# Kernel tuning notes

Measured on AMD Instinct MI355X. Metric: run time of the kernel, lower is better.

The kernel has to match this reference:

```python
import jax, jax.numpy as jnp
import numpy as np

N = 16384          # tokens (batch*seq)
D = 2048           # input_dim
H = 2 * D          # router hidden dim
E = 64             # num_experts
NUM_SHARED = 8
TOP_K = 2


def setup_inputs() -> dict:
    key = jax.random.key(0)
    k_x, k_w1, k_b1, k_w2, k_b2 = jax.random.split(key, 5)
    s1 = 1.0 / np.sqrt(D)
    s2 = 1.0 / np.sqrt(H)
    return {
        "x": jax.random.normal(k_x, (N, D), dtype=jnp.float32),
        "W1": jax.random.uniform(k_w1, (D, H), jnp.float32, -s1, s1),
        "b1": jax.random.uniform(k_b1, (H,), jnp.float32, -s1, s1),
        "W2": jax.random.uniform(k_w2, (H, E), jnp.float32, -s2, s2),
        "b2": jax.random.uniform(k_b2, (E,), jnp.float32, -s2, s2),
    }


def reference(x, W1, b1, W2, b2):
    # router MLP: linear -> exact (erf) GELU -> linear -> softmax
    h = jax.nn.gelu(x @ W1 + b1, approximate=False)          # [N, H]
    weights = jax.nn.softmax(h @ W2 + b2, axis=-1)            # [N, E]
    global_weights = weights[:, :NUM_SHARED]                  # [N, num_shared]
    local = weights[:, NUM_SHARED:]                           # [N, E - num_shared]
    local_weights, local_indices = jax.lax.top_k(local, TOP_K)  # [N, top_k] each
    return (global_weights, local_weights, local_indices, weights)
```

## Files before the change

### kernel.cpp

```cpp
#include <hip/hip_runtime.h>
#include <math.h>

namespace {
constexpr int kN = 16384;
constexpr int kD = 2048;
constexpr int kH = 4096;
constexpr int kE = 64;
constexpr int kShared = 8;

constexpr int OFF_GW = 0;
constexpr int OFF_LW = kN * kShared;
constexpr int OFF_LI = OFF_LW + kN * 2;
constexpr int OFF_W  = OFF_LI + kN * 2;

constexpr int GS_STRIDE = 132;
constexpr int HSPLIT = 4;
constexpr int CHUNKS = 8;

constexpr size_t XH_OFF  = 0;
constexpr size_t XL_OFF  = (size_t)kN * kD;
constexpr size_t W1TH_OFF = XL_OFF + (size_t)kN * kD;
constexpr size_t W1TL_OFF = W1TH_OFF + (size_t)kH * kD;
constexpr size_t WS_BASE = (W1TL_OFF + (size_t)kH * kD) * 2;
constexpr size_t PART_FLOAT_OFF = WS_BASE / 4;
constexpr size_t WS_FULL = WS_BASE + (size_t)HSPLIT * kN * kE * 4;

constexpr int BUF_FLOATS = 64 * GS_STRIDE;
constexpr int BUF_F16    = BUF_FLOATS * 2;
}

typedef _Float16 half8  __attribute__((ext_vector_type(8)));
typedef _Float16 half4t __attribute__((ext_vector_type(4)));
typedef float    f32x16 __attribute__((ext_vector_type(16)));

__device__ __forceinline__ void async16(const _Float16* g, _Float16* l) {
    __builtin_amdgcn_global_load_lds(
        (const __attribute__((address_space(1))) void*)g,
        (__attribute__((address_space(3))) void*)l, 16, 0, 0);
}

__global__ __launch_bounds__(256)
void convert_x(const float* __restrict__ x, _Float16* __restrict__ xh,
               _Float16* __restrict__ xl)
{
    const size_t i = ((size_t)blockIdx.x * 256 + threadIdx.x) * 4;
    const float4 v = *reinterpret_cast<const float4*>(x + i);
    half4t h, l;
    const float vs[4] = {v.x, v.y, v.z, v.w};
    #pragma unroll
    for (int j = 0; j < 4; ++j) {
        const _Float16 hj = (_Float16)vs[j];
        h[j] = hj;
        l[j] = (_Float16)((vs[j] - (float)hj) * 2048.0f);
    }
    *reinterpret_cast<half4t*>(xh + i) = h;
    *reinterpret_cast<half4t*>(xl + i) = l;
}

__global__ __launch_bounds__(256)
void convert_w1t(const float* __restrict__ W1, _Float16* __restrict__ th,
                 _Float16* __restrict__ tl)
{
    __shared__ float T[64][65];
    const int bk = blockIdx.x & 31;
    const int bn = blockIdx.x >> 5;
    const int k0 = bk * 64, n0 = bn * 64;
    const int t = threadIdx.x;
    const int c4 = (t & 15) * 4, r = t >> 4;

    #pragma unroll
    for (int i = 0; i < 4; ++i) {
        const int kk = r + 16 * i;
        const float4 v = *reinterpret_cast<const float4*>(
            W1 + (size_t)(k0 + kk) * kH + n0 + c4);
        T[kk][c4 + 0] = v.x; T[kk][c4 + 1] = v.y;
        T[kk][c4 + 2] = v.z; T[kk][c4 + 3] = v.w;
    }
    __syncthreads();
    #pragma unroll
    for (int i = 0; i < 4; ++i) {
        const int nn = r + 16 * i;
        half4t h, l;
        #pragma unroll
        for (int j = 0; j < 4; ++j) {
            const float vv = T[c4 + j][nn];
            const _Float16 hj = (_Float16)vv;
            h[j] = hj;
            l[j] = (_Float16)((vv - (float)hj) * 2048.0f);
        }
        *reinterpret_cast<half4t*>(th + (size_t)(n0 + nn) * kD + k0 + c4) = h;
        *reinterpret_cast<half4t*>(tl + (size_t)(n0 + nn) * kD + k0 + c4) = l;
    }
}

__global__ __launch_bounds__(256, 2)
void gemm1_mfma(const _Float16* __restrict__ xh, const float* __restrict__ b1,
                const float* __restrict__ W2, float* __restrict__ dst,
                int atomicMode)
{
    __shared__ __align__(16) float smem[2 * BUF_FLOATS];

    const int t = threadIdx.x;
    const int lane = t & 63;
    const int w = t >> 6;
    const int bx = blockIdx.x;
    const int hSplit = bx & 3;
    const int rowBlock = bx >> 2;
    const int rowBase = rowBlock * 128;

    const int mw = (w >> 1) * 64, nw = (w & 1) * 64;

    unsigned int gofsA[4], gofsB[4];
    #pragma unroll
    for (int i = 0; i < 8; ++i) {
        const int c = i * 256 + t;
        const int tile = c >> 9;
        const int s = c & 511;
        const int row = s >> 2;
        const int pq = s & 3;
        const int q = pq ^ (row & 3) ^ ((row >> 2) & 3);
        const unsigned int plane =
            (tile == 0) ? (unsigned int)XH_OFF :
            (tile == 1) ? (unsigned int)XL_OFF :
            (tile == 2) ? (unsigned int)W1TH_OFF : (unsigned int)W1TL_OFF;
        if (tile < 2)
            gofsA[i] = plane + (unsigned int)(rowBase + row) * kD + q * 8;
        else
            gofsB[i - 4] = plane + (unsigned int)row * kD + q * 8;
    }

    int aOff[2][2], bOff[2][2];
    #pragma unroll
    for (int mt = 0; mt < 2; ++mt)
        #pragma unroll
        for (int ks = 0; ks < 2; ++ks) {
            const int row = mw + mt * 32 + (lane & 31);
            const int q = (lane >> 5) + 2 * ks;
            aOff[mt][ks] = row * 32 + ((q ^ (row & 3) ^ ((row >> 2) & 3)) * 8);
        }
    #pragma unroll
    for (int nt = 0; nt < 2; ++nt)
        #pragma unroll
        for (int ks = 0; ks < 2; ++ks) {
            const int row = nw + nt * 32 + (lane & 31);
            const int q = (lane >> 5) + 2 * ks;
            bOff[nt][ks] = row * 32 + ((q ^ (row & 3) ^ ((row >> 2) & 3)) * 8);
        }

    const int g_r0 = (t >> 3) * 4;
    const int g_e0 = (t & 7) * 8;
    float lacc[4][8];
    #pragma unroll
    for (int i = 0; i < 4; ++i)
        #pragma unroll
        for (int j = 0; j < 8; ++j) lacc[i][j] = 0.0f;

    auto stage = [&](int buf, int chunk, int kt) {
        _Float16* l = (_Float16*)smem + (size_t)buf * BUF_F16;
        const unsigned int hOff =
            (unsigned int)(hSplit * (CHUNKS * 128) + chunk * 128) * kD;
        #pragma unroll
        for (int i = 0; i < 4; ++i)
            async16(xh + gofsA[i] + kt, l + ((i * 256 + t) * 8));
        #pragma unroll
        for (int i = 0; i < 4; ++i)
            async16(xh + gofsB[i] + hOff + kt, l + (((i + 4) * 256 + t) * 8));
    };

    int cur = 0;
    stage(0, 0, 0);

    for (int chunk = 0; chunk < CHUNKS; ++chunk) {
        const int hBase = hSplit * (CHUNKS * 128) + chunk * 128;

        f32x16 accH[2][2], accL[2][2];
        #pragma unroll
        for (int a = 0; a < 2; ++a)
            #pragma unroll
            for (int b = 0; b < 2; ++b)
                #pragma unroll
                for (int r = 0; r < 16; ++r) { accH[a][b][r] = 0.0f; accL[a][b][r] = 0.0f; }

        for (int kt = 0; kt < kD; kt += 32) {
            const bool isLast = (chunk == CHUNKS - 1) && (kt == kD - 32);
            if (!isLast) {
                int nc = chunk, nk = kt + 32;
                if (nk == kD) { nc = chunk + 1; nk = 0; }
                stage(cur ^ 1, nc, nk);
                asm volatile("s_waitcnt vmcnt(8)" ::: "memory");
            } else {
                asm volatile("s_waitcnt vmcnt(0)" ::: "memory");
            }
            __builtin_amdgcn_s_barrier();
            asm volatile("" ::: "memory");

            const _Float16* lds = (const _Float16*)smem + (size_t)cur * BUF_F16;

            half8 aH[2][2], aL[2][2], bH[2][2], bL[2][2];
            #pragma unroll
            for (int mt = 0; mt < 2; ++mt)
                #pragma unroll
                for (int ks = 0; ks < 2; ++ks) {
                    aH[mt][ks] = *reinterpret_cast<const half8*>(lds + aOff[mt][ks]);
                    aL[mt][ks] = *reinterpret_cast<const half8*>(lds + 4096 + aOff[mt][ks]);
                }
            #pragma unroll
            for (int nt = 0; nt < 2; ++nt)
                #pragma unroll
                for (int ks = 0; ks < 2; ++ks) {
                    bH[nt][ks] = *reinterpret_cast<const half8*>(lds + 8192 + bOff[nt][ks]);
                    bL[nt][ks] = *reinterpret_cast<const half8*>(lds + 12288 + bOff[nt][ks]);
                }

            #pragma unroll
            for (int ks = 0; ks < 2; ++ks)
                #pragma unroll
                for (int mt = 0; mt < 2; ++mt)
                    #pragma unroll
                    for (int nt = 0; nt < 2; ++nt) {
                        accH[mt][nt] = __builtin_amdgcn_mfma_f32_32x32x16_f16(
                            aH[mt][ks], bH[nt][ks], accH[mt][nt], 0, 0, 0);
                        accL[mt][nt] = __builtin_amdgcn_mfma_f32_32x32x16_f16(
                            aH[mt][ks], bL[nt][ks], accL[mt][nt], 0, 0, 0);
                        accL[mt][nt] = __builtin_amdgcn_mfma_f32_32x32x16_f16(
                            aL[mt][ks], bH[nt][ks], accL[mt][nt], 0, 0, 0);
                    }

            asm volatile("s_waitcnt lgkmcnt(0)" ::: "memory");
            __builtin_amdgcn_s_barrier();
            cur ^= 1;
        }

        float* gS = smem + (size_t)(cur ^ 1) * BUF_FLOATS;
        const float inv2048 = 1.0f / 2048.0f;
        for (int hf = 0; hf < 2; ++hf) {
            asm volatile("s_waitcnt lgkmcnt(0)" ::: "memory");
            __builtin_amdgcn_s_barrier();
            asm volatile("" ::: "memory");
            if ((w & 1) == hf) {
                #pragma unroll
                for (int nt = 0; nt < 2; ++nt) {
                    const int hl = nt * 32 + (lane & 31);
                    const float bb = b1[hBase + hf * 64 + hl];
                    #pragma unroll
                    for (int mt = 0; mt < 2; ++mt) {
                        #pragma unroll
                        for (int rq = 0; rq < 4; ++rq) {
                            float vr[4];
                            #pragma unroll
                            for (int rr = 0; rr < 4; ++rr) {
                                const int r = rq * 4 + rr;
                                const float hv = accH[mt][nt][r] + accL[mt][nt][r] * inv2048 + bb;
                                vr[rr] = 0.5f * hv * (1.0f + erff(hv * 0.70710678118654752f));
                            }
                            const int mrow = mw + mt * 32 + 8 * rq + 4 * (lane >> 5);
                            *reinterpret_cast<float4*>(gS + hl * GS_STRIDE + mrow) =
                                make_float4(vr[0], vr[1], vr[2], vr[3]);
                        }
                    }
                }
            }
            asm volatile("s_waitcnt lgkmcnt(0)" ::: "memory");
            __builtin_amdgcn_s_barrier();
            asm volatile("" ::: "memory");
            const float* W2p = W2 + (size_t)(hBase + hf * 64) * kE + g_e0;
            #pragma unroll 4
            for (int h = 0; h < 64; ++h) {
                const float4 gv = *reinterpret_cast<const float4*>(gS + h * GS_STRIDE + g_r0);
                const float4 w0 = *reinterpret_cast<const float4*>(W2p + (size_t)h * kE);
                const float4 w1 = *reinterpret_cast<const float4*>(W2p + (size_t)h * kE + 4);
                const float ga[4] = {gv.x, gv.y, gv.z, gv.w};
                const float wb[8] = {w0.x, w0.y, w0.z, w0.w, w1.x, w1.y, w1.z, w1.w};
                #pragma unroll
                for (int i = 0; i < 4; ++i)
                    #pragma unroll
                    for (int j = 0; j < 8; ++j)
                        lacc[i][j] = fmaf(ga[i], wb[j], lacc[i][j]);
            }
        }
        asm volatile("s_waitcnt lgkmcnt(0)" ::: "memory");
        __builtin_amdgcn_s_barrier();
    }

    if (atomicMode) {
        #pragma unroll
        for (int i = 0; i < 4; ++i)
            #pragma unroll
            for (int j = 0; j < 8; ++j)
                atomicAdd(dst + (size_t)(rowBase + g_r0 + i) * kE + g_e0 + j, lacc[i][j]);
    } else {
        float* drow = dst + ((size_t)hSplit * kN + rowBase + g_r0) * kE + g_e0;
        #pragma unroll
        for (int i = 0; i < 4; ++i) {
            *reinterpret_cast<float4*>(drow + (size_t)i * kE) =
                make_float4(lacc[i][0], lacc[i][1], lacc[i][2], lacc[i][3]);
            *reinterpret_cast<float4*>(drow + (size_t)i * kE + 4) =
                make_float4(lacc[i][4], lacc[i][5], lacc[i][6], lacc[i][7]);
        }
    }
}

__global__ __launch_bounds__(256, 2)
void gemm1_kernel(const float* __restrict__ x, const float* __restrict__ W1,
                  const float* __restrict__ b1, const float* __restrict__ W2,
                  float* __restrict__ logits)
{
    __shared__ __align__(16) float smem[64 * GS_STRIDE];
    float* As = smem;
    float* Bs = smem + 32 * 128;
    float* gS = smem;

    const int t  = threadIdx.x;
    const int bx = blockIdx.x;
    const int rowBlock = bx >> 2;
    const int hSplit   = bx & 3;
    const int rowBase  = rowBlock * 128;
    const int hBase0   = hSplit * 1024;

    const int ty = t >> 4;
    const int tx = t & 15;
    const int r0 = ty * 8;
    const int c0 = tx * 8;
    const int g_r0 = (t >> 3) * 4;
    const int g_e0 = (t & 7) * 8;

    float lacc[4][8];
    #pragma unroll
    for (int i = 0; i < 4; ++i)
        #pragma unroll
        for (int j = 0; j < 8; ++j) lacc[i][j] = 0.0f;

    for (int chunk = 0; chunk < 8; ++chunk) {
        const int hBase = hBase0 + chunk * 128;
        float C[8][8];
        #pragma unroll
        for (int i = 0; i < 8; ++i)
            #pragma unroll
            for (int j = 0; j < 8; ++j) C[i][j] = 0.0f;

        for (int kt = 0; kt < kD; kt += 32) {
            __syncthreads();
            #pragma unroll
            for (int i = 0; i < 4; ++i) {
                const int f  = t + 256 * i;
                const int m  = f >> 3;
                const int kq = (f & 7) * 4;
                const float4 v = *reinterpret_cast<const float4*>(
                    x + (size_t)(rowBase + m) * kD + kt + kq);
                As[(kq + 0) * 128 + m] = v.x;
                As[(kq + 1) * 128 + m] = v.y;
                As[(kq + 2) * 128 + m] = v.z;
                As[(kq + 3) * 128 + m] = v.w;
            }
            #pragma unroll
            for (int i = 0; i < 4; ++i) {
                const int f  = t + 256 * i;
                const int k  = f >> 5;
                const int n4 = (f & 31) * 4;
                *reinterpret_cast<float4*>(Bs + k * 128 + n4) =
                    *reinterpret_cast<const float4*>(W1 + (size_t)(kt + k) * kH + hBase + n4);
            }
            __syncthreads();
            #pragma unroll 8
            for (int k = 0; k < 32; ++k) {
                const float4 a0 = *reinterpret_cast<const float4*>(As + k * 128 + r0);
                const float4 a1 = *reinterpret_cast<const float4*>(As + k * 128 + r0 + 4);
                const float4 b0 = *reinterpret_cast<const float4*>(Bs + k * 128 + c0);
                const float4 b1v = *reinterpret_cast<const float4*>(Bs + k * 128 + c0 + 4);
                const float a[8] = {a0.x, a0.y, a0.z, a0.w, a1.x, a1.y, a1.z, a1.w};
                const float b[8] = {b0.x, b0.y, b0.z, b0.w, b1v.x, b1v.y, b1v.z, b1v.w};
                #pragma unroll
                for (int i = 0; i < 8; ++i)
                    #pragma unroll
                    for (int j = 0; j < 8; ++j)
                        C[i][j] = fmaf(a[i], b[j], C[i][j]);
            }
        }

        #pragma unroll
        for (int j = 0; j < 8; ++j) {
            const float bb = b1[hBase + c0 + j];
            #pragma unroll
            for (int i = 0; i < 8; ++i) {
                const float hv = C[i][j] + bb;
                C[i][j] = 0.5f * hv * (1.0f + erff(hv * 0.70710678118654752f));
            }
        }

        for (int half = 0; half < 2; ++half) {
            __syncthreads();
            if ((tx >> 3) == half) {
                const int hloc0 = c0 - half * 64;
                #pragma unroll
                for (int j = 0; j < 8; ++j) {
                    const float4 col = make_float4(C[0][j], C[1][j], C[2][j], C[3][j]);
                    const float4 col2 = make_float4(C[4][j], C[5][j], C[6][j], C[7][j]);
                    *reinterpret_cast<float4*>(gS + (hloc0 + j) * GS_STRIDE + r0)     = col;
                    *reinterpret_cast<float4*>(gS + (hloc0 + j) * GS_STRIDE + r0 + 4) = col2;
                }
            }
            __syncthreads();
            const float* W2p = W2 + (size_t)(hBase + half * 64) * kE + g_e0;
            #pragma unroll 4
            for (int h = 0; h < 64; ++h) {
                const float4 gv = *reinterpret_cast<const float4*>(gS + h * GS_STRIDE + g_r0);
                const float4 w0 = *reinterpret_cast<const float4*>(W2p + (size_t)h * kE);
                const float4 w1 = *reinterpret_cast<const float4*>(W2p + (size_t)h * kE + 4);
                const float ga[4] = {gv.x, gv.y, gv.z, gv.w};
                const float wb[8] = {w0.x, w0.y, w0.z, w0.w, w1.x, w1.y, w1.z, w1.w};
                #pragma unroll
                for (int i = 0; i < 4; ++i)
                    #pragma unroll
                    for (int j = 0; j < 8; ++j)
                        lacc[i][j] = fmaf(ga[i], wb[j], lacc[i][j]);
            }
        }
    }

    #pragma unroll
    for (int i = 0; i < 4; ++i)
        #pragma unroll
        for (int j = 0; j < 8; ++j)
            atomicAdd(logits + (size_t)(rowBase + g_r0 + i) * kE + g_e0 + j, lacc[i][j]);
}

__global__ __launch_bounds__(256)
void router_kernel(const float* __restrict__ b2, const float* __restrict__ src,
                   int atomicMode, float* __restrict__ out)
{
    const int lane = threadIdx.x & 63;
    const int row  = blockIdx.x * 4 + (threadIdx.x >> 6);

    float logit;
    if (atomicMode) {
        logit = src[(size_t)row * kE + lane] + b2[lane];
    } else {
        const float* p = src + (size_t)row * kE + lane;
        logit = p[0] + p[(size_t)kN * kE] + p[(size_t)2 * kN * kE] +
                p[(size_t)3 * kN * kE] + b2[lane];
    }

    float m = logit;
    #pragma unroll
    for (int off = 32; off > 0; off >>= 1) m = fmaxf(m, __shfl_xor(m, off));
    const float p = expf(logit - m);
    float s = p;
    #pragma unroll
    for (int off = 32; off > 0; off >>= 1) s += __shfl_xor(s, off);
    const float w = p / s;

    out[OFF_W + (size_t)row * kE + lane] = w;
    if (lane < kShared) out[OFF_GW + (size_t)row * kShared + lane] = w;

    float v1 = (lane >= kShared) ? w : -1.0f;
    int   i1 = lane - kShared;
    #pragma unroll
    for (int off = 32; off > 0; off >>= 1) {
        const float ov = __shfl_xor(v1, off);
        const int   oi = __shfl_xor(i1, off);
        if (ov > v1 || (ov == v1 && oi < i1)) { v1 = ov; i1 = oi; }
    }
    float v2 = (lane >= kShared && (lane - kShared) != i1) ? w : -1.0f;
    int   i2 = lane - kShared;
    #pragma unroll
    for (int off = 32; off > 0; off >>= 1) {
        const float ov = __shfl_xor(v2, off);
        const int   oi = __shfl_xor(i2, off);
        if (ov > v2 || (ov == v2 && oi < i2)) { v2 = ov; i2 = oi; }
    }
    if (lane == 0) {
        out[OFF_LW + (size_t)row * 2 + 0] = v1;
        out[OFF_LW + (size_t)row * 2 + 1] = v2;
        out[OFF_LI + (size_t)row * 2 + 0] = (float)i1;
        out[OFF_LI + (size_t)row * 2 + 1] = (float)i2;
    }
}

extern "C" void kernel_launch(void* const* d_in, const int* in_sizes, int n_in,
                              void* d_out, int out_size, void* d_ws, size_t ws_size,
                              hipStream_t stream)
{
    const float* x  = (const float*)d_in[0];
    const float* W1 = (const float*)d_in[1];
    const float* b1 = (const float*)d_in[2];
    const float* W2 = (const float*)d_in[3];
    const float* b2 = (const float*)d_in[4];
    float* out = (float*)d_out;
    float* logits = out + OFF_W;

    if (ws_size >= WS_BASE) {
        _Float16* base = (_Float16*)d_ws;
        const int atomicMode = (ws_size >= WS_FULL) ? 0 : 1;
        float* dst = atomicMode ? logits : ((float*)d_ws + PART_FLOAT_OFF);
        if (atomicMode)
            hipMemsetAsync(logits, 0, (size_t)kN * kE * sizeof(float), stream);
        hipLaunchKernelGGL(convert_x, dim3(kN * kD / 1024), dim3(256), 0, stream,
                           x, base + XH_OFF, base + XL_OFF);
        hipLaunchKernelGGL(convert_w1t, dim3((kD / 64) * (kH / 64)), dim3(256), 0, stream,
                           W1, base + W1TH_OFF, base + W1TL_OFF);
        hipLaunchKernelGGL(gemm1_mfma, dim3((kN / 128) * HSPLIT), dim3(256), 0, stream,
                           base + XH_OFF, b1, W2, dst, atomicMode);
        hipLaunchKernelGGL(router_kernel, dim3(kN / 4), dim3(256), 0, stream,
                           b2, dst, atomicMode, out);
    } else {
        hipMemsetAsync(logits, 0, (size_t)kN * kE * sizeof(float), stream);
        hipLaunchKernelGGL(gemm1_kernel, dim3((kN / 128) * 4), dim3(256), 0, stream,
                           x, W1, b1, W2, logits);
        hipLaunchKernelGGL(router_kernel, dim3(kN / 4), dim3(256), 0, stream,
                           b2, logits, 1, out);
    }
}
```

Measured before the change: 1.291 ms.

## Split K-step into two phases with staggered A/B prefetch and interleaved N mapping

Each 32-wide K step is split into two 16-wide halves, each with its own LDS fragment loads and MFMA group. The A-tile prefetch is issued before the first half and the B-tile prefetch after the second half's fragment reads, with s_setprio raised around the MFMA groups. This is meant to overlap global loads with compute and reduce register pressure. The warp N mapping is changed so each warp holds interleaved 32-column slices, which lets every warp run the GELU epilogue for both halves instead of idling half the warps. The cost is an extra barrier per K step and more delicate vmcnt and LDS-hazard sequencing.

```diff
diff --git a/kernel.cpp b/kernel.cpp
--- a/kernel.cpp
+++ b/kernel.cpp
@@ -108,7 +108,8 @@
     const int rowBlock = bx >> 2;
     const int rowBase = rowBlock * 128;
 
-    const int mw = (w >> 1) * 64, nw = (w & 1) * 64;
+    const int mw = (w >> 1) * 64;
+    const int nc32 = (w & 1) * 32;
 
     unsigned int gofsA[4], gofsB[4];
     #pragma unroll
@@ -142,7 +143,7 @@
     for (int nt = 0; nt < 2; ++nt)
         #pragma unroll
         for (int ks = 0; ks < 2; ++ks) {
-            const int row = nw + nt * 32 + (lane & 31);
+            const int row = nt * 64 + nc32 + (lane & 31);
             const int q = (lane >> 5) + 2 * ks;
             bOff[nt][ks] = row * 32 + ((q ^ (row & 3) ^ ((row >> 2) & 3)) * 8);
         }
@@ -155,20 +156,24 @@
         #pragma unroll
         for (int j = 0; j < 8; ++j) lacc[i][j] = 0.0f;
 
-    auto stage = [&](int buf, int chunk, int kt) {
+    auto stageA = [&](int buf, int nk) {
+        _Float16* l = (_Float16*)smem + (size_t)buf * BUF_F16;
+        #pragma unroll
+        for (int i = 0; i < 4; ++i)
+            async16(xh + gofsA[i] + nk, l + ((i * 256 + t) * 8));
+    };
+    auto stageB = [&](int buf, int nc, int nk) {
         _Float16* l = (_Float16*)smem + (size_t)buf * BUF_F16;
         const unsigned int hOff =
-            (unsigned int)(hSplit * (CHUNKS * 128) + chunk * 128) * kD;
+            (unsigned int)(hSplit * (CHUNKS * 128) + nc * 128) * kD;
         #pragma unroll
         for (int i = 0; i < 4; ++i)
-            async16(xh + gofsA[i] + kt, l + ((i * 256 + t) * 8));
-        #pragma unroll
-        for (int i = 0; i < 4; ++i)
-            async16(xh + gofsB[i] + hOff + kt, l + (((i + 4) * 256 + t) * 8));
+            async16(xh + gofsB[i] + hOff + nk, l + (((i + 4) * 256 + t) * 8));
     };
 
     int cur = 0;
-    stage(0, 0, 0);
+    stageA(0, 0);
+    stageB(0, 0, 0);
 
     for (int chunk = 0; chunk < CHUNKS; ++chunk) {
         const int hBase = hSplit * (CHUNKS * 128) + chunk * 128;
@@ -183,81 +188,110 @@
 
         for (int kt = 0; kt < kD; kt += 32) {
             const bool isLast = (chunk == CHUNKS - 1) && (kt == kD - 32);
+            int nc = chunk, nk = kt + 32;
+            if (nk == kD) { nc = chunk + 1; nk = 0; }
+
+            const _Float16* lds = (const _Float16*)smem + (size_t)cur * BUF_F16;
+            const int nbuf = cur ^ 1;
+
             if (!isLast) {
-                int nc = chunk, nk = kt + 32;
-                if (nk == kD) { nc = chunk + 1; nk = 0; }
-                stage(cur ^ 1, nc, nk);
-                asm volatile("s_waitcnt vmcnt(8)" ::: "memory");
+                stageA(nbuf, nk);
+                asm volatile("s_waitcnt vmcnt(4)" ::: "memory");
             } else {
                 asm volatile("s_waitcnt vmcnt(0)" ::: "memory");
             }
             __builtin_amdgcn_s_barrier();
             asm volatile("" ::: "memory");
 
-            const _Float16* lds = (const _Float16*)smem + (size_t)cur * BUF_F16;
-
-            half8 aH[2][2], aL[2][2], bH[2][2], bL[2][2];
-            #pragma unroll
-            for (int mt = 0; mt < 2; ++mt)
-                #pragma unroll
-                for (int ks = 0; ks < 2; ++ks) {
-                    aH[mt][ks] = *reinterpret_cast<const half8*>(lds + aOff[mt][ks]);
-                    aL[mt][ks] = *reinterpret_cast<const half8*>(lds + 4096 + aOff[mt][ks]);
+            {
+                half8 aH[2], aL[2], bH[2], bL[2];
+                #pragma unroll
+                for (int mt = 0; mt < 2; ++mt) {
+                    aH[mt] = *reinterpret_cast<const half8*>(lds + aOff[mt][0]);
+                    aL[mt] = *reinterpret_cast<const half8*>(lds + 4096 + aOff[mt][0]);
                 }
-            #pragma unroll
-            for (int nt = 0; nt < 2; ++nt)
-                #pragma unroll
-                for (int ks = 0; ks < 2; ++ks) {
-                    bH[nt][ks] = *reinterpret_cast<const half8*>(lds + 8192 + bOff[nt][ks]);
-                    bL[nt][ks] = *reinterpret_cast<const half8*>(lds + 12288 + bOff[nt][ks]);
+                #pragma unroll
+                for (int nt = 0; nt < 2; ++nt) {
+                    bH[nt] = *reinterpret_cast<const half8*>(lds + 8192 + bOff[nt][0]);
+                    bL[nt] = *reinterpret_cast<const half8*>(lds + 12288 + bOff[nt][0]);
                 }
-
-            #pragma unroll
-            for (int ks = 0; ks < 2; ++ks)
+                __builtin_amdgcn_s_setprio(1);
                 #pragma unroll
                 for (int mt = 0; mt < 2; ++mt)
                     #pragma unroll
                     for (int nt = 0; nt < 2; ++nt) {
                         accH[mt][nt] = __builtin_amdgcn_mfma_f32_32x32x16_f16(
-                            aH[mt][ks], bH[nt][ks], accH[mt][nt], 0, 0, 0);
+                            aH[mt], bH[nt], accH[mt][nt], 0, 0, 0);
                         accL[mt][nt] = __builtin_amdgcn_mfma_f32_32x32x16_f16(
-                            aH[mt][ks], bL[nt][ks], accL[mt][nt], 0, 0, 0);
+                            aH[mt], bL[nt], accL[mt][nt], 0, 0, 0);
                         accL[mt][nt] = __builtin_amdgcn_mfma_f32_32x32x16_f16(
-                            aL[mt][ks], bH[nt][ks], accL[mt][nt], 0, 0, 0);
+                            aL[mt], bH[nt], accL[mt][nt], 0, 0, 0);
                     }
-
-            asm volatile("s_waitcnt lgkmcnt(0)" ::: "memory");
+                __builtin_amdgcn_s_setprio(0);
+                __builtin_amdgcn_sched_barrier(0);
+            }
+            asm volatile("" ::: "memory");
             __builtin_amdgcn_s_barrier();
-            cur ^= 1;
-        }
-
-        float* gS = smem + (size_t)(cur ^ 1) * BUF_FLOATS;
-        const float inv2048 = 1.0f / 2048.0f;
-        for (int hf = 0; hf < 2; ++hf) {
+            asm volatile("" ::: "memory");
+
+            {
+                half8 aH[2], aL[2], bH[2], bL[2];
+                #pragma unroll
+                for (int mt = 0; mt < 2; ++mt) {
+                    aH[mt] = *reinterpret_cast<const half8*>(lds + aOff[mt][1]);
+                    aL[mt] = *reinterpret_cast<const half8*>(lds + 4096 + aOff[mt][1]);
+                }
+                #pragma unroll
+                for (int nt = 0; nt < 2; ++nt) {
+                    bH[nt] = *reinterpret_cast<const half8*>(lds + 8192 + bOff[nt][1]);
+                    bL[nt] = *reinterpret_cast<const half8*>(lds + 12288 + bOff[nt][1]);
+                }
+                if (!isLast) stageB(nbuf, nc, nk);
+                __builtin_amdgcn_s_setprio(1);
+                #pragma unroll
+                for (int mt = 0; mt < 2; ++mt)
+                    #pragma unroll
+                    for (int nt = 0; nt < 2; ++nt) {
+                        accH[mt][nt] = __builtin_amdgcn_mfma_f32_32x32x16_f16(
+                            aH[mt], bH[nt], accH[mt][nt], 0, 0, 0);
+                        accL[mt][nt] = __builtin_amdgcn_mfma_f32_32x32x16_f16(
+                            aH[mt], bL[nt], accL[mt][nt], 0, 0, 0);
+                        accL[mt][nt] = __builtin_amdgcn_mfma_f32_32x32x16_f16(
+                            aL[mt], bH[nt], accL[mt][nt], 0, 0, 0);
+                    }
+                __builtin_amdgcn_s_setprio(0);
+                __builtin_amdgcn_sched_barrier(0);
+            }
             asm volatile("s_waitcnt lgkmcnt(0)" ::: "memory");
             __builtin_amdgcn_s_barrier();
             asm volatile("" ::: "memory");
-            if ((w & 1) == hf) {
-                #pragma unroll
-                for (int nt = 0; nt < 2; ++nt) {
-                    const int hl = nt * 32 + (lane & 31);
-                    const float bb = b1[hBase + hf * 64 + hl];
+            cur ^= 1;
+        }
+
+        float* gS = smem + (size_t)(cur ^ 1) * BUF_FLOATS;
+        const float inv2048 = 1.0f / 2048.0f;
+        const int hl = nc32 + (lane & 31);
+        for (int hf = 0; hf < 2; ++hf) {
+            if (hf) {
+                asm volatile("s_waitcnt lgkmcnt(0)" ::: "memory");
+                __builtin_amdgcn_s_barrier();
+                asm volatile("" ::: "memory");
+            }
+            const float bb = b1[hBase + hf * 64 + hl];
+            #pragma unroll
+            for (int mt = 0; mt < 2; ++mt) {
+                #pragma unroll
+                for (int rq = 0; rq < 4; ++rq) {
+                    float vr[4];
                     #pragma unroll
-                    for (int mt = 0; mt < 2; ++mt) {
-                        #pragma unroll
-                        for (int rq = 0; rq < 4; ++rq) {
-                            float vr[4];
-                            #pragma unroll
-                            for (int rr = 0; rr < 4; ++rr) {
-                                const int r = rq * 4 + rr;
-                                const float hv = accH[mt][nt][r] + accL[mt][nt][r] * inv2048 + bb;
-                                vr[rr] = 0.5f * hv * (1.0f + erff(hv * 0.70710678118654752f));
-                            }
-                            const int mrow = mw + mt * 32 + 8 * rq + 4 * (lane >> 5);
-                            *reinterpret_cast<float4*>(gS + hl * GS_STRIDE + mrow) =
-                                make_float4(vr[0], vr[1], vr[2], vr[3]);
-                        }
+                    for (int rr = 0; rr < 4; ++rr) {
+                        const int r = rq * 4 + rr;
+                        const float hv = accH[mt][hf][r] + accL[mt][hf][r] * inv2048 + bb;
+                        vr[rr] = 0.5f * hv * (1.0f + erff(hv * 0.70710678118654752f));
                     }
+                    const int mrow = mw + mt * 32 + 8 * rq + 4 * (lane >> 5);
+                    *reinterpret_cast<float4*>(gS + hl * GS_STRIDE + mrow) =
+                        make_float4(vr[0], vr[1], vr[2], vr[3]);
                 }
             }
             asm volatile("s_waitcnt lgkmcnt(0)" ::: "memory");
@@ -280,6 +314,7 @@
         }
         asm volatile("s_waitcnt lgkmcnt(0)" ::: "memory");
         __builtin_amdgcn_s_barrier();
+        asm volatile("" ::: "memory");
     }
 
     if (atomicMode) {
```

Result: faster. 1.247 ms (-3.5%).
